# Optimization experiments

Measured on AMD Instinct MI355X. Metric: run time of the kernel, lower is better.

Reference implementation:

```python
import jax, jax.numpy as jnp
import numpy as np
from jax.scipy.linalg import cholesky, solve_triangular, cho_solve

N, M, D = 16384, 2048, 8
VAR, LS = 1.0, 0.5      # RBF kernel hyperparameters (same for kernel_f and kernel_g)
JITTER = 1e-6
BATCH_RATE = 1.0
HALF_LOG_2PI = 0.5 * float(np.log(2.0 * np.pi))


def rbf(x1, x2):
    # K[i,j] = VAR * exp(-||x1_i - x2_j||^2 / (2 LS^2))
    d2 = (jnp.sum(x1 * x1, 1)[:, None] + jnp.sum(x2 * x2, 1)[None, :]
          - 2.0 * (x1 @ x2.T))
    return VAR * jnp.exp(-0.5 * d2 / (LS * LS))


def setup_inputs() -> dict:
    key = jax.random.key(0)
    ks = jax.random.split(key, 7)
    x = jax.random.normal(ks[0], (N, D), dtype=jnp.float32)
    y = jax.random.normal(ks[1], (N, 1), dtype=jnp.float32)
    z = 2.0 * jax.random.uniform(ks[2], (M, D), dtype=jnp.float32) - 1.0  # inducing inputs in [-1,1]^D
    q_m_f = 0.5 * jax.random.normal(ks[3], (M, 1), dtype=jnp.float32)
    q_m_g = 0.5 * jax.random.normal(ks[4], (M, 1), dtype=jnp.float32)
    # Cholesky-like params: identity plus small strictly-lower noise -> PD covariance
    q_L_f = jnp.eye(M, dtype=jnp.float32) + 0.01 * jnp.tril(
        jax.random.normal(ks[5], (M, M), dtype=jnp.float32), -1)
    q_L_g = jnp.eye(M, dtype=jnp.float32) + 0.01 * jnp.tril(
        jax.random.normal(ks[6], (M, M), dtype=jnp.float32), -1)
    return {"x": x, "y": y, "z": z, "q_m_f": q_m_f, "q_L_f": q_L_f,
            "q_m_g": q_m_g, "q_L_g": q_L_g}


def _gp_marginals_and_kl(x, z, q_m, q_L_raw):
    """Marginal posterior mean/var at x and KL(q(u)||p(u)) for one sparse GP."""
    L_S = jnp.tril(q_L_raw)                     # [M,M]
    Kuu = rbf(z, z) + JITTER * jnp.eye(M, dtype=x.dtype)
    Lk = cholesky(Kuu, lower=True)
    Kfu = rbf(x, z)                             # [N,M]
    # A = Kfu @ Kuu^{-1}
    A = cho_solve((Lk, True), Kfu.T).T          # [N,M]
    m = (A @ q_m)[:, 0]                         # [N]
    # diag(Kff + A (S - Kuu) A^T) = diag(Kff) + diag(A S A^T) - diag(Kfu A^T)
    S = L_S @ L_S.T
    diag_Kff = jnp.full((x.shape[0],), VAR, dtype=x.dtype)
    v = diag_Kff + jnp.sum((A @ S) * A, axis=1) - jnp.sum(A * Kfu, axis=1)
    # KL(N(q_m, S) || N(0, Kuu))
    alpha = solve_triangular(Lk, q_m, lower=True)       # Kuu^{-1/2} m
    W = solve_triangular(Lk, L_S, lower=True)           # Kuu^{-1/2} L_S
    logdet_K = 2.0 * jnp.sum(jnp.log(jnp.diag(Lk)))
    logdet_S = 2.0 * jnp.sum(jnp.log(jnp.abs(jnp.diag(L_S))))
    kl = 0.5 * (jnp.sum(W * W) + jnp.sum(alpha * alpha)
                - jnp.asarray(M, x.dtype) + logdet_K - logdet_S)
    return m, v, kl


def reference(x, y, z, q_m_f, q_L_f, q_m_g, q_L_g):
    m_f, v_f, kl_f = _gp_marginals_and_kl(x, z, q_m_f, q_L_f)
    m_g, v_g, kl_g = _gp_marginals_and_kl(x, z, q_m_g, q_L_g)
    yv = y[:, 0]
    # HetGaussian variational expectation (Saul et al. 2016):
    # E_q[log N(y | f, exp(g))] per point
    expectation = (-HALF_LOG_2PI - 0.5 * m_g
                   - 0.5 * ((yv - m_f) ** 2 + v_f) * jnp.exp(-m_g + 0.5 * v_g))
    elbo = BATCH_RATE * jnp.sum(expectation) - (kl_f + kl_g)
    return -elbo
```

## Files before the change

kernel.cpp:

```cpp
#include <hip/hip_runtime.h>
#include <math.h>

#define NN 16384
#define MM 2048
#define DD 8
#define NB 32
#define SZB ((size_t)16777216)

constexpr float HLOG2PI = 0.91893853320467274178f;

using short8  = __attribute__((ext_vector_type(8))) short;
using float4v = __attribute__((ext_vector_type(4))) float;

__device__ __forceinline__ float4v f4zero(){ float4v v; v[0]=0.f; v[1]=0.f; v[2]=0.f; v[3]=0.f; return v; }

__device__ __forceinline__ void bfsplit(float v, short& h, short& lo){
  unsigned b = __float_as_uint(v);
  h = (short)(b >> 16);
  float hf = __uint_as_float(b & 0xFFFF0000u);
  lo = (short)(__float_as_uint(v - hf) >> 16);
}
__device__ __forceinline__ float bf2f(short s){
  return __uint_as_float(((unsigned)(unsigned short)s) << 16);
}
__device__ __forceinline__ float4v mfma3(short8 ah, short8 al, short8 bh, short8 bl, float4v c){
  c = __builtin_amdgcn_mfma_f32_16x16x32_bf16(ah, bh, c, 0, 0, 0);
  c = __builtin_amdgcn_mfma_f32_16x16x32_bf16(ah, bl, c, 0, 0, 0);
  c = __builtin_amdgcn_mfma_f32_16x16x32_bf16(al, bh, c, 0, 0, 0);
  return c;
}

__device__ __forceinline__ float block_reduce(float v, float* scratch){
  int lane = threadIdx.x & 63;
  int w    = threadIdx.x >> 6;
  #pragma unroll
  for (int off=32; off; off>>=1) v += __shfl_down(v, off, 64);
  __syncthreads();
  if (lane==0) scratch[w] = v;
  __syncthreads();
  float r = 0.f;
  if (threadIdx.x < 4) r = scratch[threadIdx.x];
  if (w==0){ r += __shfl_down(r, 2, 64); r += __shfl_down(r, 1, 64); }
  return r;
}

__device__ __forceinline__ void stage64(float (*S)[68], const float* __restrict__ g, int ld, int t){
  #pragma unroll
  for (int p=t; p<1024; p+=256)
    *(float4*)&S[p>>4][(p&15)*4] = *(const float4*)&g[(size_t)(p>>4)*ld + (p&15)*4];
}
__device__ __forceinline__ void tile_gemm_step(float acc[4][4], const float (*As)[68], const float (*Bs)[68], int tx, int ty){
  for (int k=0;k<64;++k){
    float ar[4], bc4[4];
    #pragma unroll
    for (int u=0;u<4;++u){ ar[u]=As[ty*4+u][k]; bc4[u]=Bs[k][tx*4+u]; }
    #pragma unroll
    for (int u=0;u<4;++u)
      #pragma unroll
      for (int v=0;v<4;++v) acc[u][v] += ar[u]*bc4[v];
  }
}
__device__ __forceinline__ void tile_syrk_step(float acc[4][4], const float (*P)[68], const float (*Q)[68], int tx, int ty){
  for (int k=0;k<64;++k){
    float pr[4], qc[4];
    #pragma unroll
    for (int u=0;u<4;++u){ pr[u]=P[ty*4+u][k]; qc[u]=Q[tx*4+u][k]; }
    #pragma unroll
    for (int u=0;u<4;++u)
      #pragma unroll
      for (int v=0;v<4;++v) acc[u][v] += pr[u]*qc[v];
  }
}

__device__ __forceinline__ void factor64_reg(const float (*S)[68],
    float* __restrict__ lkd, float* __restrict__ sdg_, int d, int t){
  if (t < 64){
    float xr[64];
    #pragma unroll
    for (int c4=0;c4<16;++c4) *(float4*)&xr[c4*4] = *(const float4*)&S[t][c4*4];
    float myrp = 1.f;
    #pragma unroll
    for (int j=0;j<64;++j){
      float ajj = __shfl(xr[j], j, 64);
      float piv = sqrtf(fmaxf(ajj, 1e-20f));
      float rp  = 1.f/piv;
      float val = xr[j]*rp;
      if (t==j){ xr[j] = piv; myrp = rp; }
      else if (t>j) xr[j] = val;
      else val = 0.f;
      #pragma unroll
      for (int c=j+1;c<64;++c){
        float vc = __shfl(val, c, 64);
        if (c<=t) xr[c] -= val*vc;
      }
    }
    #pragma unroll
    for (int c=0;c<64;++c) if (c>t) xr[c] = 0.f;
    #pragma unroll
    for (int c4=0;c4<16;++c4)
      *(float4*)&lkd[d*4096 + t*64 + c4*4] = *(float4*)&xr[c4*4];
    sdg_[d*64 + t] = myrp;
  }
}


__global__ __launch_bounds__(256) void phase0_kernel(
    const float* __restrict__ z, float* __restrict__ kuu,
    short* __restrict__ zfh, short* __restrict__ zfl, float* __restrict__ zn2,
    float* __restrict__ lkdiag, float* __restrict__ sdg){
  __shared__ float As[64][68];
  __shared__ float Bs[64][68];
  const int t = threadIdx.x, tx = t & 15, ty = t >> 4;
  const int bid = blockIdx.x;
  if (bid >= 528){
    int zr = (bid-528)*256 + t;
    float v[DD]; float s = 0.f;
    #pragma unroll
    for (int d=0; d<DD; ++d){ v[d] = z[zr*DD + d]; s += v[d]*v[d]; }
    zn2[zr] = s;
    size_t base = (size_t)(zr >> 4)*512 + (zr & 15)*32;
    #pragma unroll
    for (int k=0; k<32; ++k){
      short h = 0, lo = 0;
      if (k < DD) bfsplit(v[k], h, lo);
      zfh[base + k] = h; zfl[base + k] = lo;
    }
    return;
  }
  int idx = bid;
  int r=0; while ((r+1)*(r+2)/2 <= idx) ++r;
  int c = idx - r*(r+1)/2;
  for (int p=t; p<128; p+=256){ int i=p>>1, h=p&1;
    *(float4*)&As[i][h*4] = *(const float4*)&z[(size_t)(r*64+i)*DD + h*4];
    *(float4*)&Bs[i][h*4] = *(const float4*)&z[(size_t)(c*64+i)*DD + h*4]; }
  __syncthreads();
  float kv[4][4];
  #pragma unroll
  for (int u=0;u<4;++u)
    #pragma unroll
    for (int v=0;v<4;++v){
      float d2=0.f;
      #pragma unroll
      for (int d=0;d<8;++d){ float df=As[ty*4+u][d]-Bs[tx*4+v][d]; d2+=df*df; }
      float val = __expf(-2.f*d2);
      if (r*64+ty*4+u == c*64+tx*4+v) val += 1e-6f;
      kv[u][v] = val;
    }
  #pragma unroll
  for (int u=0;u<4;++u)
    *(float4*)&kuu[(size_t)(r*64+ty*4+u)*MM + c*64 + tx*4] =
        make_float4(kv[u][0],kv[u][1],kv[u][2],kv[u][3]);
  if (idx == 0){
    __syncthreads();
    #pragma unroll
    for (int u=0;u<4;++u)
      #pragma unroll
      for (int v=0;v<4;++v) As[ty*4+u][tx*4+v] = kv[u][v];
    __syncthreads();
    factor64_reg(As, lkdiag, sdg, 0, t);
  }
}

__global__ __launch_bounds__(256) void panel_kernel(
    float* __restrict__ kuu, float* __restrict__ lkdiag,
    float* __restrict__ sdg, float* __restrict__ ltri, int kb){
  __shared__ float As[64][68];
  __shared__ float Bs[64][68];
  __shared__ float Cs[64][68];
  __shared__ float sd[64];
  const int t = threadIdx.x, tx = t & 15, ty = t >> 4;
  int idx = blockIdx.x;
  int r=0; while ((r+1)*(r+2)/2 <= idx) ++r;
  int c = idx - r*(r+1)/2;
  int bi = kb+1+r, bc = kb+1+c;
  stage64(Cs, lkdiag + kb*4096, 64, t);
  if (t < 64) sd[t] = sdg[kb*64 + t];
  stage64(As, kuu + (size_t)(bi*64)*MM + kb*64, MM, t);
  if (bc != bi) stage64(Bs, kuu + (size_t)(bc*64)*MM + kb*64, MM, t);
  __syncthreads();
  {
    int w = t>>6, l = t&63;
    if (w==0 || (w==1 && bc!=bi)){
      float (*S)[68] = (w==0)? As : Bs;
      float xr[64];
      #pragma unroll
      for (int c4=0;c4<16;++c4) *(float4*)&xr[c4*4] = *(const float4*)&S[l][c4*4];
      #pragma unroll
      for (int j=0;j<64;++j){
        float xj = xr[j]*sd[j];
        xr[j] = xj;
        #pragma unroll
        for (int cc=j+1;cc<64;++cc) xr[cc] -= xj*Cs[cc][j];
      }
      #pragma unroll
      for (int c4=0;c4<16;++c4) *(float4*)&S[l][c4*4] = *(float4*)&xr[c4*4];
    }
  }
  __syncthreads();
  if (bc == kb+1){
    for (int p=t;p<1024;p+=256)
      *(float4*)&ltri[(size_t)(bi*64+(p>>4))*MM + kb*64 + (p&15)*4] =
          *(float4*)&As[p>>4][(p&15)*4];
  }
  float acc[4][4] = {};
  tile_syrk_step(acc, As, (bc==bi)? As : Bs, tx, ty);
  if (bi==kb+1 && bc==kb+1){
    __syncthreads();
    #pragma unroll
    for (int u=0;u<4;++u)
      #pragma unroll
      for (int v=0;v<4;++v) Bs[ty*4+u][tx*4+v] = acc[u][v];
    __syncthreads();
    for (int p=t;p<1024;p+=256){
      int i=p>>4, c4=p&15;
      float4 kv = *(const float4*)&kuu[(size_t)(bi*64+i)*MM + bi*64 + c4*4];
      float4 bv = *(float4*)&Bs[i][c4*4];
      float4 o; o.x=kv.x-bv.x; o.y=kv.y-bv.y; o.z=kv.z-bv.z; o.w=kv.w-bv.w;
      *(float4*)&As[i][c4*4] = o;
    }
    __syncthreads();
    factor64_reg(As, lkdiag, sdg, kb+1, t);
  } else {
    #pragma unroll
    for (int u=0;u<4;++u){
      float4* dst = (float4*)&kuu[(size_t)(bi*64+ty*4+u)*MM + bc*64 + tx*4];
      float4 o = *dst;
      o.x-=acc[u][0]; o.y-=acc[u][1]; o.z-=acc[u][2]; o.w-=acc[u][3];
      *dst = o;
    }
  }
}

__global__ __launch_bounds__(256) void panel30_phase2_kernel(
    float* __restrict__ kuu, float* __restrict__ lkdiag,
    float* __restrict__ sdg, float* __restrict__ ltri, float* __restrict__ linv){
  __shared__ float As[64][68];
  __shared__ float Bs[64][68];
  __shared__ float Cs[64][68];
  __shared__ float sd[64];
  const int t = threadIdx.x, tx = t & 15, ty = t >> 4;
  const int bid = blockIdx.x;
  int d;
  if (bid == 0){
    const int kb = 30, bi = 31;
    stage64(Cs, lkdiag + kb*4096, 64, t);
    if (t < 64) sd[t] = sdg[kb*64 + t];
    stage64(As, kuu + (size_t)(bi*64)*MM + kb*64, MM, t);
    __syncthreads();
    {
      int w = t>>6, l = t&63;
      if (w==0){
        float xr[64];
        #pragma unroll
        for (int c4=0;c4<16;++c4) *(float4*)&xr[c4*4] = *(const float4*)&As[l][c4*4];
        #pragma unroll
        for (int j=0;j<64;++j){
          float xj = xr[j]*sd[j];
          xr[j] = xj;
          #pragma unroll
          for (int cc=j+1;cc<64;++cc) xr[cc] -= xj*Cs[cc][j];
        }
        #pragma unroll
        for (int c4=0;c4<16;++c4) *(float4*)&As[l][c4*4] = *(float4*)&xr[c4*4];
      }
    }
    __syncthreads();
    for (int p=t;p<1024;p+=256)
      *(float4*)&ltri[(size_t)(bi*64+(p>>4))*MM + kb*64 + (p&15)*4] =
          *(float4*)&As[p>>4][(p&15)*4];
    float acc[4][4] = {};
    tile_syrk_step(acc, As, As, tx, ty);
    __syncthreads();
    #pragma unroll
    for (int u=0;u<4;++u)
      #pragma unroll
      for (int v=0;v<4;++v) Bs[ty*4+u][tx*4+v] = acc[u][v];
    __syncthreads();
    for (int p=t;p<1024;p+=256){
      int i=p>>4, c4=p&15;
      float4 kv = *(const float4*)&kuu[(size_t)(bi*64+i)*MM + bi*64 + c4*4];
      float4 bv = *(float4*)&Bs[i][c4*4];
      float4 o; o.x=kv.x-bv.x; o.y=kv.y-bv.y; o.z=kv.z-bv.z; o.w=kv.w-bv.w;
      *(float4*)&As[i][c4*4] = o;
    }
    __syncthreads();
    factor64_reg(As, lkdiag, sdg, 31, t);
    __syncthreads();
    d = 31;
  } else {
    d = bid - 1;
  }
  stage64(As, lkdiag + d*4096, 64, t);
  __syncthreads();
  if (t < 64){
    for (int j=0;j<64;++j){
      float s = (j==t)?1.f:0.f;
      for (int k=t;k<j;++k) s -= As[j][k]*Bs[k][t];
      Bs[j][t] = (j>=t)? s/As[j][j] : 0.f;
    }
  }
  __syncthreads();
  for (int p=t;p<1024;p+=256){ int i=p>>4, c4=p&15;
    *(float4*)&linv[(size_t)(d*64+i)*MM + d*64 + c4*4] = *(float4*)&Bs[i][c4*4]; }
}

__global__ __launch_bounds__(256) void p3l0_kernel(
    const float* __restrict__ ltri, float* __restrict__ linv){
  __shared__ float As[64][68];
  __shared__ float Bs[64][68];
  const int t = threadIdx.x, tx = t & 15, ty = t >> 4;
  int m = blockIdx.x;
  stage64(As, ltri + (size_t)((2*m+1)*64)*MM + (2*m)*64, MM, t);
  stage64(Bs, linv + (size_t)((2*m)*64)*MM   + (2*m)*64, MM, t);
  __syncthreads();
  float acc[4][4]={};
  tile_gemm_step(acc, As, Bs, tx, ty);
  __syncthreads();
  #pragma unroll
  for (int u=0;u<4;++u)
    #pragma unroll
    for (int v=0;v<4;++v) Bs[ty*4+u][tx*4+v] = acc[u][v];
  stage64(As, linv + (size_t)((2*m+1)*64)*MM + (2*m+1)*64, MM, t);
  __syncthreads();
  float o[4][4]={};
  tile_gemm_step(o, As, Bs, tx, ty);
  #pragma unroll
  for (int u=0;u<4;++u)
    *(float4*)&linv[(size_t)((2*m+1)*64+ty*4+u)*MM + (2*m)*64 + tx*4] =
        make_float4(-o[u][0],-o[u][1],-o[u][2],-o[u][3]);
}

__global__ __launch_bounds__(256) void p3l1_kernel(
    const float* __restrict__ ltri, float* __restrict__ linv, float* __restrict__ ptmp){
  __shared__ float As[64][68];
  __shared__ float Bs[64][68];
  const int t = threadIdx.x, tx = t & 15, ty = t >> 4;
  int m = blockIdx.x;
  float* pm = ptmp + (size_t)m*128*128;
  for (int ti=0; ti<2; ++ti)
    for (int tj=0; tj<2; ++tj){
      int rb = m*4 + 2 + ti, cb0 = m*4;
      float acc[4][4]={};
      for (int k=tj; k<2; ++k){
        __syncthreads();
        stage64(As, ltri + (size_t)(rb*64)*MM + (cb0+k)*64, MM, t);
        stage64(Bs, linv + (size_t)((cb0+k)*64)*MM + (cb0+tj)*64, MM, t);
        __syncthreads();
        tile_gemm_step(acc, As, Bs, tx, ty);
      }
      #pragma unroll
      for (int u=0;u<4;++u)
        *(float4*)&pm[(size_t)(ti*64+ty*4+u)*128 + tj*64 + tx*4] =
            make_float4(acc[u][0],acc[u][1],acc[u][2],acc[u][3]);
    }
  for (int ti=0; ti<2; ++ti)
    for (int tj=0; tj<2; ++tj){
      int rb = m*4 + 2 + ti;
      float acc[4][4]={};
      for (int k=0; k<=ti; ++k){
        __syncthreads();
        stage64(As, linv + (size_t)(rb*64)*MM + (m*4+2+k)*64, MM, t);
        stage64(Bs, pm + (size_t)(k*64)*128 + tj*64, 128, t);
        __syncthreads();
        tile_gemm_step(acc, As, Bs, tx, ty);
      }
      #pragma unroll
      for (int u=0;u<4;++u)
        *(float4*)&linv[(size_t)(rb*64+ty*4+u)*MM + (m*4+tj)*64 + tx*4] =
            make_float4(-acc[u][0],-acc[u][1],-acc[u][2],-acc[u][3]);
    }
}

__global__ __launch_bounds__(256) void p3lA_kernel(
    const float* __restrict__ ltri, const float* __restrict__ linv,
    float* __restrict__ ptmp, int s){
  __shared__ float As[64][68];
  __shared__ float Bs[64][68];
  const int t = threadIdx.x, tx = t & 15, ty = t >> 4;
  int nb = 1<<s, b = 64<<s;
  float* pmb = ptmp + (s==2 ? 131072 : (s==3 ? 393216 : 917504));
  int idx = blockIdx.x;
  int m = idx/(nb*nb), r2 = idx%(nb*nb);
  int ti = r2/nb, tj = r2%nb;
  int rb = m*2*nb + nb + ti, cb0 = m*2*nb;
  float acc[4][4]={};
  for (int k=tj; k<nb; ++k){
    __syncthreads();
    stage64(As, ltri + (size_t)(rb*64)*MM + (cb0+k)*64, MM, t);
    stage64(Bs, linv + (size_t)((cb0+k)*64)*MM + (cb0+tj)*64, MM, t);
    __syncthreads();
    tile_gemm_step(acc, As, Bs, tx, ty);
  }
  float* pm = pmb + (size_t)m*b*b;
  #pragma unroll
  for (int u=0;u<4;++u)
    *(float4*)&pm[(size_t)(ti*64+ty*4+u)*b + tj*64 + tx*4] =
        make_float4(acc[u][0],acc[u][1],acc[u][2],acc[u][3]);
}

__global__ __launch_bounds__(256) void p3lB_kernel(
    float* __restrict__ linv, const float* __restrict__ ptmp, int s){
  __shared__ float As[64][68];
  __shared__ float Bs[64][68];
  const int t = threadIdx.x, tx = t & 15, ty = t >> 4;
  int nb = 1<<s, b = 64<<s;
  const float* pmb = ptmp + (s==2 ? 131072 : (s==3 ? 393216 : 917504));
  int idx = blockIdx.x;
  int m = idx/(nb*nb), r2 = idx%(nb*nb);
  int ti = r2/nb, tj = r2%nb;
  int rb = m*2*nb + nb + ti;
  const float* pm = pmb + (size_t)m*b*b;
  float acc[4][4]={};
  for (int k=0; k<=ti; ++k){
    __syncthreads();
    stage64(As, linv + (size_t)(rb*64)*MM + (m*2*nb+nb+k)*64, MM, t);
    stage64(Bs, pm + (size_t)(k*64)*b + tj*64, b, t);
    __syncthreads();
    tile_gemm_step(acc, As, Bs, tx, ty);
  }
  #pragma unroll
  for (int u=0;u<4;++u)
    *(float4*)&linv[(size_t)(rb*64+ty*4+u)*MM + (m*2*nb+tj)*64 + tx*4] =
        make_float4(-acc[u][0],-acc[u][1],-acc[u][2],-acc[u][3]);
}

__global__ __launch_bounds__(256) void walpha_split_kernel(
    const float* __restrict__ linv, const float* __restrict__ qlf,
    const float* __restrict__ qlg, const float* __restrict__ qmf,
    const float* __restrict__ qmg, float* __restrict__ wf, float* __restrict__ wg,
    float* __restrict__ af, float* __restrict__ ag,
    short* __restrict__ lvh, short* __restrict__ lvl){
  __shared__ float As[64][68];
  __shared__ float Bs[64][68];
  const int t = threadIdx.x, tx = t & 15, ty = t >> 4;
  int idx = blockIdx.x;
  if (idx >= 1312){
    int p = (idx-1312)*256 + t;
    int chunk = p >> 9, wi = p & 511;
    int mo = chunk >> 6, ko = chunk & 63;
    int row = mo*16 + (wi >> 5), col = ko*32 + (wi & 31);
    float v = linv[(size_t)row*MM + col];
    short h, lo; bfsplit(v, h, lo);
    lvh[p] = h; lvl[p] = lo;
    return;
  }
  if (idx >= 1056){
    int abid = idx - 1056;
    int gw = abid*4 + (t>>6), l = t&63;
    for (int job=gw; job<4096; job+=1024){
      int gp = job>>11, r = job&2047;
      const float* qm = gp ? qmg : qmf;
      float s=0.f;
      for (int c=l; c<=r; c+=64) s += linv[(size_t)r*MM+c]*qm[c];
      #pragma unroll
      for (int off=32; off; off>>=1) s += __shfl_down(s, off, 64);
      if (l==0) (gp ? ag : af)[r] = s;
    }
    return;
  }
  int gp = idx/528, rem = idx%528;
  int bi=0; while ((bi+1)*(bi+2)/2 <= rem) ++bi;
  int bj = rem - bi*(bi+1)/2;
  const float* ql = gp ? qlg : qlf;
  float* w        = gp ? wg  : wf;
  float acc[4][4]={};
  for (int bk=bj; bk<=bi; ++bk){
    __syncthreads();
    stage64(As, linv + (size_t)(bi*64)*MM + bk*64, MM, t);
    stage64(Bs, ql   + (size_t)(bk*64)*MM + bj*64, MM, t);
    __syncthreads();
    if (bk==bj){
      for (int p=t;p<4096;p+=256){ int i=p>>6, c=p&63; if (i<c) Bs[i][c]=0.f; }
      __syncthreads();
    }
    tile_gemm_step(acc, As, Bs, tx, ty);
  }
  #pragma unroll
  for (int u=0;u<4;++u)
    *(float4*)&w[(size_t)(bi*64+ty*4+u)*MM + bj*64 + tx*4] =
        make_float4(acc[u][0],acc[u][1],acc[u][2],acc[u][3]);
}

__global__ __launch_bounds__(256) void reduce_kernel(
    const float* __restrict__ lkd, const float* __restrict__ qlf,
    const float* __restrict__ qlg, const float* __restrict__ af,
    const float* __restrict__ ag, const float* __restrict__ wf,
    const float* __restrict__ wg, float* __restrict__ scal){
  __shared__ float scratch[4];
  if (blockIdx.x == 512){
    float ldk=0, ldf=0, ldg=0, a2f=0, a2g=0;
    for (int i=threadIdx.x;i<MM;i+=256){
      int kb = i>>6, r = i&63;
      ldk += __logf(lkd[kb*4096 + r*64 + r]);
      ldf += __logf(fabsf(qlf[(size_t)i*MM+i]));
      ldg += __logf(fabsf(qlg[(size_t)i*MM+i]));
      float v = af[i]; a2f += v*v;
      v = ag[i];       a2g += v*v;
    }
    float r;
    r = block_reduce(ldk, scratch); if (threadIdx.x==0) scal[0] = 2.f*r;
    r = block_reduce(ldf, scratch); if (threadIdx.x==0) scal[1] = 2.f*r;
    r = block_reduce(ldg, scratch); if (threadIdx.x==0) scal[2] = 2.f*r;
    r = block_reduce(a2f, scratch); if (threadIdx.x==0) scal[3] = r;
    r = block_reduce(a2g, scratch); if (threadIdx.x==0) scal[4] = r;
    return;
  }
  size_t start  = (size_t)blockIdx.x*256 + threadIdx.x;
  size_t stride = (size_t)512*256;
  float sf=0, sg=0;
  for (size_t p=start;p<(size_t)MM*MM;p+=stride){
    float v=wf[p]; sf += v*v;
    v=wg[p];       sg += v*v;
  }
  float r = block_reduce(sf, scratch);
  if (threadIdx.x==0) atomicAdd(&scal[5], r);
  r = block_reduce(sg, scratch);
  if (threadIdx.x==0) atomicAdd(&scal[6], r);
}

__global__ __launch_bounds__(256, 2) void split_tt_kernel(
    const float* __restrict__ wf, const float* __restrict__ wg,
    short* __restrict__ wfh, short* __restrict__ wfl,
    short* __restrict__ wgh, short* __restrict__ wgl,
    const float* __restrict__ x, const float* __restrict__ zn2,
    const short* __restrict__ zfh, const short* __restrict__ zfl,
    const short* __restrict__ lvh, const short* __restrict__ lvl,
    short* __restrict__ tth, short* __restrict__ ttl){
  __shared__ __align__(16) short lAh[8192], lAl[8192], lBh[8192], lBl[8192];
  __shared__ float tile[32][33];
  const int t = threadIdx.x;
  const int bid = blockIdx.x;
  if (bid < 8192){
    int zz = bid >> 12;
    int rem = bid & 4095;
    int mb = rem & 63, kb = rem >> 6;
    const float* src = zz ? wg : wf;
    short* dh = zz ? wgh : wfh;
    short* dl = zz ? wgl : wfl;
    #pragma unroll
    for (int k=0;k<4;++k){
      int idx = t + k*256;
      int lr = idx >> 5, lc = idx & 31;
      tile[lr][lc] = src[(size_t)(kb*32+lr)*MM + mb*32 + lc];
    }
    __syncthreads();
    #pragma unroll
    for (int e=0;e<4;++e){
      int p = t*4 + e;
      int c = p >> 9, wi = p & 511;
      int i = (wi >> 5) & 15, kk = wi & 31;
      float v = tile[kk][c*16 + i];
      short h, lo; bfsplit(v, h, lo);
      size_t gp = ((size_t)(mb*2 + c)*64 + kb)*512 + wi;
      dh[gp] = h; dl[gp] = lo;
    }
    return;
  }
  int v0 = bid - 8192;
  int istrip = v0 % 128, bj2 = v0 / 128;
  int l = t & 63, w = t >> 6;
  int li = l & 15, q = l >> 4;
  int lofs = li*32 + q*8;
  int lofs_s = li*32 + ((q ^ ((li>>1)&3)))*8;
  int wn4 = (w>>1)*4, wm4 = (w&1)*4;

  short8 xh[2], xl[2];
  float xn2v[8];
  {
    float xn2t[2];
    #pragma unroll
    for (int tn=0; tn<2; ++tn){
      int n = istrip*128 + w*32 + tn*16 + li;
      const float4* xp = (const float4*)(x + (size_t)n*DD);
      float4 p0 = xp[0], p1 = xp[1];
      float v[8] = {p0.x,p0.y,p0.z,p0.w,p1.x,p1.y,p1.z,p1.w};
      float s = 0.f;
      #pragma unroll
      for (int d=0; d<8; ++d) s += v[d]*v[d];
      xn2t[tn] = s;
      short8 hh, ll;
      #pragma unroll
      for (int j=0; j<8; ++j){
        short h=0, lo=0;
        if (q==0) bfsplit(v[j], h, lo);
        hh[j]=h; ll[j]=lo;
      }
      xh[tn]=hh; xl[tn]=ll;
    }
    #pragma unroll
    for (int tn=0; tn<2; ++tn)
      #pragma unroll
      for (int r=0; r<4; ++r)
        xn2v[tn*4+r] = __shfl(xn2t[tn], q*4 + r, 64);
  }

  float4v acc[4][4];
  #pragma unroll
  for (int i=0;i<4;++i)
    #pragma unroll
    for (int j=0;j<4;++j) acc[i][j] = f4zero();

  int nkt = 2*bj2 + 2;
  for (int bk=0; bk<nkt; ++bk){
    __syncthreads();
    {
      short8 zh[4], zl[4];
      float zt2[4];
      #pragma unroll
      for (int tz=0; tz<4; ++tz){
        size_t zo = (size_t)(bk*4 + tz)*512 + lofs;
        zh[tz] = *(const short8*)(zfh + zo);
        zl[tz] = *(const short8*)(zfl + zo);
        zt2[tz] = zn2[bk*64 + tz*16 + li];
      }
      #pragma unroll
      for (int tn=0; tn<2; ++tn){
        #pragma unroll
        for (int tz=0; tz<4; ++tz){
          float4v s4 = mfma3(xh[tn], xl[tn], zh[tz], zl[tz], f4zero());
          #pragma unroll
          for (int r=0; r<4; ++r){
            float e = __expf(4.f*s4[r] - 2.f*(xn2v[tn*4+r] + zt2[tz]));
            short h, lo; bfsplit(e, h, lo);
            int rowc = q*4 + r;
            int slot2 = (((tz&1)*2 + (li>>3)) ^ ((rowc>>1)&3));
            int pos = ((w*2+tn)*2 + (tz>>1))*512 + rowc*32 + slot2*8 + (li&7);
            lAh[pos] = h; lAl[pos] = lo;
          }
        }
      }
    }
    #pragma unroll
    for (int c4 = t; c4 < 1024; c4 += 256){
      int ch = c4 >> 6, wdi = c4 & 63;
      int wsw = (wdi & 60) | ((wdi ^ (wdi >> 3)) & 3);
      int dst = ch*64 + wsw;
      size_t g = ((size_t)(bj2*8 + (ch>>1))*64 + (size_t)(bk*2 + (ch&1)))*64 + wdi;
      ((uint4*)lBh)[dst] = ((const uint4*)lvh)[g];
      ((uint4*)lBl)[dst] = ((const uint4*)lvl)[g];
    }
    __syncthreads();
    #pragma unroll
    for (int s=0; s<2; ++s){
      short8 ah[4], al[4], bh[4], bl[4];
      #pragma unroll
      for (int tn=0; tn<4; ++tn){
        int off = ((wn4+tn)*2 + s)*512 + lofs_s;
        ah[tn] = *(const short8*)&lAh[off];
        al[tn] = *(const short8*)&lAl[off];
      }
      #pragma unroll
      for (int tm=0; tm<4; ++tm){
        int off = ((wm4+tm)*2 + s)*512 + lofs_s;
        bh[tm] = *(const short8*)&lBh[off];
        bl[tm] = *(const short8*)&lBl[off];
      }
      #pragma unroll
      for (int tn=0; tn<4; ++tn)
        #pragma unroll
        for (int tm=0; tm<4; ++tm)
          acc[tn][tm] = mfma3(ah[tn], al[tn], bh[tm], bl[tm], acc[tn][tm]);
    }
  }
  #pragma unroll
  for (int tn=0; tn<4; ++tn){
    int no_g = istrip*8 + wn4 + tn;
    #pragma unroll
    for (int tm=0; tm<4; ++tm){
      int mo_g = bj2*4 + (w&1)*2 + (tm>>1);
      size_t cb = ((size_t)no_g*64 + mo_g)*512;
      #pragma unroll
      for (int r=0; r<4; ++r){
        short h, lo; bfsplit(acc[tn][tm][r], h, lo);
        size_t pos = cb + (q*4+r)*32 + (tm&1)*16 + li;
        tth[pos] = h; ttl[pos] = lo;
      }
    }
  }
}

__global__ __launch_bounds__(256, 2) void linquadkl_kernel(
    const short* __restrict__ tth, const short* __restrict__ ttl,
    const float* __restrict__ af, const float* __restrict__ ag,
    float* __restrict__ t2, float* __restrict__ lf, float* __restrict__ lg,
    const short* __restrict__ wfh, const short* __restrict__ wfl,
    const short* __restrict__ wgh, const short* __restrict__ wgl,
    float* __restrict__ vfq, float* __restrict__ vgq,
    const float* __restrict__ scal, float* __restrict__ out){
  __shared__ __align__(16) short lAh[8192], lAl[8192], lBh[8192], lBl[8192];
  const int t = threadIdx.x;
  const int bid = blockIdx.x;
  if (bid == 8192){
    if (t == 0){
      float klf = 0.5f*(scal[5] + scal[3] - (float)MM + scal[0] - scal[1]);
      float klg = 0.5f*(scal[6] + scal[4] - (float)MM + scal[0] - scal[2]);
      out[0] += klf + klg;
    }
    return;
  }
  if (bid < 4096){
    int w = t >> 6, l = t & 63;
    int n = bid*4 + w;
    int g = l >> 2, j = l & 3;
    float s2=0.f, sf=0.f, sg=0.f;
    #pragma unroll
    for (int it=0; it<4; ++it){
      int ck = g + it*16;
      size_t off = ((size_t)(n>>4)*64 + ck)*512 + (n&15)*32 + j*8;
      short8 h8 = *(const short8*)(tth + off);
      short8 l8 = *(const short8*)(ttl + off);
      int m0 = ck*32 + j*8;
      float4 a0 = *(const float4*)(af + m0), a1 = *(const float4*)(af + m0 + 4);
      float4 g0 = *(const float4*)(ag + m0), g1 = *(const float4*)(ag + m0 + 4);
      float av[8] = {a0.x,a0.y,a0.z,a0.w,a1.x,a1.y,a1.z,a1.w};
      float gv[8] = {g0.x,g0.y,g0.z,g0.w,g1.x,g1.y,g1.z,g1.w};
      #pragma unroll
      for (int e=0; e<8; ++e){
        float tv = bf2f(h8[e]) + bf2f(l8[e]);
        s2 += tv*tv; sf += tv*av[e]; sg += tv*gv[e];
      }
    }
    #pragma unroll
    for (int off=32; off; off>>=1){
      s2 += __shfl_down(s2, off, 64);
      sf += __shfl_down(sf, off, 64);
      sg += __shfl_down(sg, off, 64);
    }
    if (l==0){ t2[n] = s2; lf[n] = sf; lg[n] = sg; }
    return;
  }
  int v0 = bid - 4096;
  int istrip = v0 % 128, bj2 = (v0 / 128) % 16, zz = v0 / 2048;
  int l = t & 63, w = t >> 6;
  const short* gbh = zz ? wgh : wfh;
  const short* gbl = zz ? wgl : wfl;
  float* vq = zz ? vgq : vfq;
  int li = l & 15, q = l >> 4;
  int lofs_s = li*32 + ((q ^ ((li>>1)&3)))*8;
  int wn4 = (w>>1)*4, wm4 = (w&1)*4;

  float4v acc[4][4];
  #pragma unroll
  for (int i=0;i<4;++i)
    #pragma unroll
    for (int j=0;j<4;++j) acc[i][j] = f4zero();

  for (int bk=2*bj2; bk<32; ++bk){
    __syncthreads();
    #pragma unroll
    for (int c4 = t; c4 < 1024; c4 += 256){
      int ch = c4 >> 6, wdi = c4 & 63;
      int wsw = (wdi & 60) | ((wdi ^ (wdi >> 3)) & 3);
      int dst = ch*64 + wsw;
      size_t ga = ((size_t)(istrip*8 + (ch>>1))*64 + (size_t)(bk*2 + (ch&1)))*64 + wdi;
      ((uint4*)lAh)[dst] = ((const uint4*)tth)[ga];
      ((uint4*)lAl)[dst] = ((const uint4*)ttl)[ga];
      size_t gb = ((size_t)(bj2*8 + (ch>>1))*64 + (size_t)(bk*2 + (ch&1)))*64 + wdi;
      ((uint4*)lBh)[dst] = ((const uint4*)gbh)[gb];
      ((uint4*)lBl)[dst] = ((const uint4*)gbl)[gb];
    }
    __syncthreads();
    #pragma unroll
    for (int s=0; s<2; ++s){
      short8 ah[4], al[4], bh[4], bl[4];
      #pragma unroll
      for (int tn=0; tn<4; ++tn){
        int off = ((wn4+tn)*2 + s)*512 + lofs_s;
        ah[tn] = *(const short8*)&lAh[off];
        al[tn] = *(const short8*)&lAl[off];
      }
      #pragma unroll
      for (int tm=0; tm<4; ++tm){
        int off = ((wm4+tm)*2 + s)*512 + lofs_s;
        bh[tm] = *(const short8*)&lBh[off];
        bl[tm] = *(const short8*)&lBl[off];
      }
      #pragma unroll
      for (int tn=0; tn<4; ++tn)
        #pragma unroll
        for (int tm=0; tm<4; ++tm)
          acc[tn][tm] = mfma3(ah[tn], al[tn], bh[tm], bl[tm], acc[tn][tm]);
    }
  }
  float rs[16];
  #pragma unroll
  for (int tn=0; tn<4; ++tn)
    #pragma unroll
    for (int r=0; r<4; ++r){
      float s = 0.f;
      #pragma unroll
      for (int tm=0; tm<4; ++tm){ float v = acc[tn][tm][r]; s += v*v; }
      rs[tn*4+r] = s;
    }
  #pragma unroll
  for (int off=8; off; off>>=1)
    #pragma unroll
    for (int k=0; k<16; ++k) rs[k] += __shfl_down(rs[k], off, 16);
  if (li == 0){
    #pragma unroll
    for (int tn=0; tn<4; ++tn)
      #pragma unroll
      for (int r=0; r<4; ++r){
        int n = istrip*128 + (w>>1)*64 + tn*16 + q*4 + r;
        atomicAdd(&vq[n], rs[tn*4+r]);
      }
  }
}

__global__ __launch_bounds__(256) void final_kernel(const float* __restrict__ y,
    const float* __restrict__ t2, const float* __restrict__ lf, const float* __restrict__ lg,
    const float* __restrict__ vfq, const float* __restrict__ vgq, float* __restrict__ out){
  __shared__ float scratch[4];
  int i = blockIdx.x*256 + threadIdx.x;
  float mf = lf[i], mg = lg[i];
  float vf = 1.f + vfq[i] - t2[i];
  float vg = 1.f + vgq[i] - t2[i];
  float dy = y[i] - mf;
  float e = -HLOG2PI - 0.5f*mg - 0.5f*(dy*dy + vf)*__expf(-mg + 0.5f*vg);
  float r = block_reduce(e, scratch);
  if (threadIdx.x==0) atomicAdd(out, -r);
}

extern "C" void kernel_launch(void* const* d_in, const int* in_sizes, int n_in,
                              void* d_out, int out_size, void* d_ws, size_t ws_size,
                              hipStream_t stream){
  (void)in_sizes; (void)n_in; (void)out_size; (void)ws_size;
  const float* x   = (const float*)d_in[0];
  const float* y   = (const float*)d_in[1];
  const float* z   = (const float*)d_in[2];
  const float* qmf = (const float*)d_in[3];
  const float* qlf = (const float*)d_in[4];
  const float* qmg = (const float*)d_in[5];
  const float* qlg = (const float*)d_in[6];
  float* out = (float*)d_out;
  char* Bw = (char*)d_ws;

  float* kuu  = (float*)Bw;
  float* linv = (float*)(Bw + SZB);
  float* wf   = (float*)(Bw + 2*SZB);
  float* wg   = (float*)(Bw + 3*SZB);
  short* lvh  = (short*)Bw;
  short* lvl  = (short*)(Bw + SZB/2);
  short* wfh  = (short*)(Bw + SZB);
  short* wfl  = (short*)(Bw + SZB + SZB/2);
  short* wgh  = (short*)(Bw + 2*SZB);
  short* wgl  = (short*)(Bw + 2*SZB + SZB/2);
  short* tth  = (short*)(Bw + 3*SZB);
  short* ttl  = (short*)(Bw + 3*SZB + (size_t)NN*MM*2);
  float* ltri   = (float*)(Bw + 4*SZB);
  float* ptmp   = (float*)(Bw + 5*SZB);
  float* lkdiag = (float*)(Bw + 5*SZB + (size_t)8388608);
  float* sdg    = (float*)(Bw + 5*SZB + (size_t)8388608 + (size_t)524288);
  float* sm   = (float*)(Bw + 3*SZB + (size_t)NN*MM*4);
  float* af = sm;          float* ag = af + MM;
  float* t2 = ag + MM;     float* lf = t2 + NN;   float* lg = lf + NN;
  float* vfq = lg + NN;    float* vgq = vfq + NN; float* scal = vgq + NN;
  float* zn2 = scal + 64 + 2048;
  short* zfh = (short*)(zn2 + MM);
  short* zfl = zfh + MM*32;

  hipMemsetAsync(out, 0, sizeof(float), stream);
  hipMemsetAsync(vfq, 0, (size_t)(2*NN + 64 + 2048)*sizeof(float), stream);
  hipMemsetAsync(wf,  0, 2*SZB, stream);
  hipMemsetAsync(linv,0, SZB,   stream);

  phase0_kernel<<<536, 256, 0, stream>>>(z, kuu, zfh, zfl, zn2, lkdiag, sdg);
  for (int kb = 0; kb < 30; ++kb){
    int T = NB - 1 - kb;
    panel_kernel<<<T*(T+1)/2, 256, 0, stream>>>(kuu, lkdiag, sdg, ltri, kb);
  }
  panel30_phase2_kernel<<<32, 256, 0, stream>>>(kuu, lkdiag, sdg, ltri, linv);
  p3l0_kernel<<<16, 256, 0, stream>>>(ltri, linv);
  p3l1_kernel<<<8, 256, 0, stream>>>(ltri, linv, ptmp);
  for (int s = 2; s < 5; ++s){
    int nb = 1<<s, mc = 16>>s;
    p3lA_kernel<<<mc*nb*nb, 256, 0, stream>>>(ltri, linv, ptmp, s);
    p3lB_kernel<<<mc*nb*nb, 256, 0, stream>>>(linv, ptmp, s);
  }
  walpha_split_kernel<<<17696, 256, 0, stream>>>(linv, qlf, qlg, qmf, qmg,
                                                 wf, wg, af, ag, lvh, lvl);
  reduce_kernel<<<513, 256, 0, stream>>>(lkdiag, qlf, qlg, af, ag, wf, wg, scal);
  split_tt_kernel<<<10240, 256, 0, stream>>>(wf, wg, wfh, wfl, wgh, wgl,
                                             x, zn2, zfh, zfl, lvh, lvl, tth, ttl);
  linquadkl_kernel<<<8193, 256, 0, stream>>>(tth, ttl, af, ag, t2, lf, lg,
                                             wfh, wfl, wgh, wgl, vfq, vgq, scal, out);
  final_kernel<<<NN/256, 256, 0, stream>>>(y, t2, lf, lg, vfq, vgq, out);
}
```

Baseline: 3.827 ms.

## Fuse two Cholesky panel steps per launch to halve kernel launches

Replaces the 30 per-column-block panel launches of the blocked Cholesky with 15 launches, each handling two 64-wide column blocks. Every block redundantly factors the second diagonal block and applies both trailing updates before writing back. This removes half of the serialized launches and one global read-modify-write of the trailing matrix per pair. In exchange each block does redundant factorization work and uses more shared memory (six 64x68 tiles), which may reduce occupancy.

```diff
diff --git a/kernel.cpp b/kernel.cpp
--- a/kernel.cpp
+++ b/kernel.cpp
@@ -70,6 +70,20 @@
       #pragma unroll
       for (int v=0;v<4;++v) acc[u][v] += pr[u]*qc[v];
   }
+}
+__device__ __forceinline__ void trsm_row(float* Srow, const float (*C)[68], const float* sdv){
+  float xr[64];
+  #pragma unroll
+  for (int c4=0;c4<16;++c4) *(float4*)&xr[c4*4] = *(const float4*)&Srow[c4*4];
+  #pragma unroll
+  for (int j=0;j<64;++j){
+    float xj = xr[j]*sdv[j];
+    xr[j] = xj;
+    #pragma unroll
+    for (int cc=j+1;cc<64;++cc) xr[cc] -= xj*C[cc][j];
+  }
+  #pragma unroll
+  for (int c4=0;c4<16;++c4) *(float4*)&Srow[c4*4] = *(float4*)&xr[c4*4];
 }
 
 __device__ __forceinline__ void factor64_reg(const float (*S)[68],
@@ -100,6 +114,42 @@
     for (int c4=0;c4<16;++c4)
       *(float4*)&lkd[d*4096 + t*64 + c4*4] = *(float4*)&xr[c4*4];
     sdg_[d*64 + t] = myrp;
+  }
+}
+
+__device__ __forceinline__ void factor64_ip(float (*S)[68], float* sdl,
+    float* __restrict__ lkd, float* __restrict__ sdg_, int d, int t, bool glob){
+  if (t < 64){
+    float xr[64];
+    #pragma unroll
+    for (int c4=0;c4<16;++c4) *(float4*)&xr[c4*4] = *(const float4*)&S[t][c4*4];
+    float myrp = 1.f;
+    #pragma unroll
+    for (int j=0;j<64;++j){
+      float ajj = __shfl(xr[j], j, 64);
+      float piv = sqrtf(fmaxf(ajj, 1e-20f));
+      float rp  = 1.f/piv;
+      float val = xr[j]*rp;
+      if (t==j){ xr[j] = piv; myrp = rp; }
+      else if (t>j) xr[j] = val;
+      else val = 0.f;
+      #pragma unroll
+      for (int c=j+1;c<64;++c){
+        float vc = __shfl(val, c, 64);
+        if (c<=t) xr[c] -= val*vc;
+      }
+    }
+    #pragma unroll
+    for (int c=0;c<64;++c) if (c>t) xr[c] = 0.f;
+    #pragma unroll
+    for (int c4=0;c4<16;++c4) *(float4*)&S[t][c4*4] = *(float4*)&xr[c4*4];
+    sdl[t] = myrp;
+    if (glob){
+      #pragma unroll
+      for (int c4=0;c4<16;++c4)
+        *(float4*)&lkd[d*4096 + t*64 + c4*4] = *(float4*)&xr[c4*4];
+      sdg_[d*64 + t] = myrp;
+    }
   }
 }
 
@@ -161,71 +211,112 @@
   }
 }
 
-__global__ __launch_bounds__(256) void panel_kernel(
+__global__ __launch_bounds__(256) void panel2_kernel(
     float* __restrict__ kuu, float* __restrict__ lkdiag,
-    float* __restrict__ sdg, float* __restrict__ ltri, int kb){
+    float* __restrict__ sdg, float* __restrict__ ltri, int p){
   __shared__ float As[64][68];
   __shared__ float Bs[64][68];
+  __shared__ float A1s[64][68];
+  __shared__ float B1s[64][68];
   __shared__ float Cs[64][68];
-  __shared__ float sd[64];
+  __shared__ float Ds[64][68];
+  __shared__ float sd[64], sd2[64];
   const int t = threadIdx.x, tx = t & 15, ty = t >> 4;
+  const int d0 = 2*p, d1 = 2*p+1, rs = 2*p+2;
   int idx = blockIdx.x;
   int r=0; while ((r+1)*(r+2)/2 <= idx) ++r;
   int c = idx - r*(r+1)/2;
-  int bi = kb+1+r, bc = kb+1+c;
-  stage64(Cs, lkdiag + kb*4096, 64, t);
-  if (t < 64) sd[t] = sdg[kb*64 + t];
-  stage64(As, kuu + (size_t)(bi*64)*MM + kb*64, MM, t);
-  if (bc != bi) stage64(Bs, kuu + (size_t)(bc*64)*MM + kb*64, MM, t);
+  int bi = rs + r, bc = rs + c;
+  const bool dual = (bc != bi);
+  stage64(Cs, lkdiag + d0*4096, 64, t);
+  if (t < 64) sd[t] = sdg[d0*64 + t];
+  stage64(As, kuu + (size_t)(bi*64)*MM + d0*64, MM, t);
+  if (dual) stage64(Bs, kuu + (size_t)(bc*64)*MM + d0*64, MM, t);
+  stage64(Ds, kuu + (size_t)(d1*64)*MM + d0*64, MM, t);
   __syncthreads();
   {
     int w = t>>6, l = t&63;
-    if (w==0 || (w==1 && bc!=bi)){
-      float (*S)[68] = (w==0)? As : Bs;
-      float xr[64];
-      #pragma unroll
-      for (int c4=0;c4<16;++c4) *(float4*)&xr[c4*4] = *(const float4*)&S[l][c4*4];
-      #pragma unroll
-      for (int j=0;j<64;++j){
-        float xj = xr[j]*sd[j];
-        xr[j] = xj;
-        #pragma unroll
-        for (int cc=j+1;cc<64;++cc) xr[cc] -= xj*Cs[cc][j];
-      }
-      #pragma unroll
-      for (int c4=0;c4<16;++c4) *(float4*)&S[l][c4*4] = *(float4*)&xr[c4*4];
-    }
-  }
-  __syncthreads();
-  if (bc == kb+1){
-    for (int p=t;p<1024;p+=256)
-      *(float4*)&ltri[(size_t)(bi*64+(p>>4))*MM + kb*64 + (p&15)*4] =
-          *(float4*)&As[p>>4][(p&15)*4];
-  }
-  float acc[4][4] = {};
-  tile_syrk_step(acc, As, (bc==bi)? As : Bs, tx, ty);
-  if (bi==kb+1 && bc==kb+1){
-    __syncthreads();
+    float (*S)[68] = (w==0) ? As : ((w==1 && dual) ? Bs : ((w==2) ? Ds : (float(*)[68])nullptr));
+    if (S) trsm_row(&S[l][0], (const float (*)[68])Cs, sd);
+  }
+  __syncthreads();
+  if (bc == rs){
+    for (int q=t;q<1024;q+=256)
+      *(float4*)&ltri[(size_t)(bi*64+(q>>4))*MM + d0*64 + (q&15)*4] =
+          *(float4*)&As[q>>4][(q&15)*4];
+  }
+  if (idx == 0){
+    for (int q=t;q<1024;q+=256)
+      *(float4*)&ltri[(size_t)(d1*64+(q>>4))*MM + d0*64 + (q&15)*4] =
+          *(float4*)&Ds[q>>4][(q&15)*4];
+  }
+  {
+    float accd[4][4] = {};
+    tile_syrk_step(accd, (const float (*)[68])Ds, (const float (*)[68])Ds, tx, ty);
+    #pragma unroll
+    for (int u=0;u<4;++u){
+      float4 kv = *(const float4*)&kuu[(size_t)(d1*64+ty*4+u)*MM + d1*64 + tx*4];
+      Cs[ty*4+u][tx*4  ] = kv.x - accd[u][0];
+      Cs[ty*4+u][tx*4+1] = kv.y - accd[u][1];
+      Cs[ty*4+u][tx*4+2] = kv.z - accd[u][2];
+      Cs[ty*4+u][tx*4+3] = kv.w - accd[u][3];
+    }
+  }
+  __syncthreads();
+  factor64_ip(Cs, sd2, lkdiag, sdg, d1, t, (idx==0));
+  stage64(A1s, kuu + (size_t)(bi*64)*MM + d1*64, MM, t);
+  if (dual) stage64(B1s, kuu + (size_t)(bc*64)*MM + d1*64, MM, t);
+  __syncthreads();
+  {
+    float aA[4][4]={}, aB[4][4]={};
+    tile_syrk_step(aA, (const float (*)[68])As, (const float (*)[68])Ds, tx, ty);
+    if (dual) tile_syrk_step(aB, (const float (*)[68])Bs, (const float (*)[68])Ds, tx, ty);
     #pragma unroll
     for (int u=0;u<4;++u)
       #pragma unroll
-      for (int v=0;v<4;++v) Bs[ty*4+u][tx*4+v] = acc[u][v];
-    __syncthreads();
-    for (int p=t;p<1024;p+=256){
-      int i=p>>4, c4=p&15;
-      float4 kv = *(const float4*)&kuu[(size_t)(bi*64+i)*MM + bi*64 + c4*4];
-      float4 bv = *(float4*)&Bs[i][c4*4];
-      float4 o; o.x=kv.x-bv.x; o.y=kv.y-bv.y; o.z=kv.z-bv.z; o.w=kv.w-bv.w;
-      *(float4*)&As[i][c4*4] = o;
-    }
-    __syncthreads();
-    factor64_reg(As, lkdiag, sdg, kb+1, t);
+      for (int v=0;v<4;++v){
+        A1s[ty*4+u][tx*4+v] -= aA[u][v];
+        if (dual) B1s[ty*4+u][tx*4+v] -= aB[u][v];
+      }
+  }
+  __syncthreads();
+  {
+    int w = t>>6, l = t&63;
+    float (*S)[68] = (w==0) ? A1s : ((w==1 && dual) ? B1s : (float(*)[68])nullptr);
+    if (S) trsm_row(&S[l][0], (const float (*)[68])Cs, sd2);
+  }
+  __syncthreads();
+  if (bc == rs){
+    for (int q=t;q<1024;q+=256)
+      *(float4*)&ltri[(size_t)(bi*64+(q>>4))*MM + d1*64 + (q&15)*4] =
+          *(float4*)&A1s[q>>4][(q&15)*4];
+  }
+  float acc0[4][4]={}, acc1[4][4]={};
+  tile_syrk_step(acc0, (const float (*)[68])As,  dual ? (const float (*)[68])Bs  : (const float (*)[68])As,  tx, ty);
+  tile_syrk_step(acc1, (const float (*)[68])A1s, dual ? (const float (*)[68])B1s : (const float (*)[68])A1s, tx, ty);
+  if (idx == 0){
+    __syncthreads();
+    #pragma unroll
+    for (int u=0;u<4;++u){
+      float4 kv = *(const float4*)&kuu[(size_t)(rs*64+ty*4+u)*MM + rs*64 + tx*4];
+      float x0 = kv.x - acc0[u][0]; x0 -= acc1[u][0];
+      float x1 = kv.y - acc0[u][1]; x1 -= acc1[u][1];
+      float x2 = kv.z - acc0[u][2]; x2 -= acc1[u][2];
+      float x3 = kv.w - acc0[u][3]; x3 -= acc1[u][3];
+      Bs[ty*4+u][tx*4  ] = x0;
+      Bs[ty*4+u][tx*4+1] = x1;
+      Bs[ty*4+u][tx*4+2] = x2;
+      Bs[ty*4+u][tx*4+3] = x3;
+    }
+    __syncthreads();
+    factor64_reg((const float (*)[68])Bs, lkdiag, sdg, rs, t);
   } else {
     #pragma unroll
     for (int u=0;u<4;++u){
       float4* dst = (float4*)&kuu[(size_t)(bi*64+ty*4+u)*MM + bc*64 + tx*4];
       float4 o = *dst;
-      o.x-=acc[u][0]; o.y-=acc[u][1]; o.z-=acc[u][2]; o.w-=acc[u][3];
+      o.x-=acc0[u][0]; o.y-=acc0[u][1]; o.z-=acc0[u][2]; o.w-=acc0[u][3];
+      o.x-=acc1[u][0]; o.y-=acc1[u][1]; o.z-=acc1[u][2]; o.w-=acc1[u][3];
       *dst = o;
     }
   }
@@ -249,27 +340,14 @@
     __syncthreads();
     {
       int w = t>>6, l = t&63;
-      if (w==0){
-        float xr[64];
-        #pragma unroll
-        for (int c4=0;c4<16;++c4) *(float4*)&xr[c4*4] = *(const float4*)&As[l][c4*4];
-        #pragma unroll
-        for (int j=0;j<64;++j){
-          float xj = xr[j]*sd[j];
-          xr[j] = xj;
-          #pragma unroll
-          for (int cc=j+1;cc<64;++cc) xr[cc] -= xj*Cs[cc][j];
-        }
-        #pragma unroll
-        for (int c4=0;c4<16;++c4) *(float4*)&As[l][c4*4] = *(float4*)&xr[c4*4];
-      }
+      if (w==0) trsm_row(&As[l][0], (const float (*)[68])Cs, sd);
     }
     __syncthreads();
     for (int p=t;p<1024;p+=256)
       *(float4*)&ltri[(size_t)(bi*64+(p>>4))*MM + kb*64 + (p&15)*4] =
           *(float4*)&As[p>>4][(p&15)*4];
     float acc[4][4] = {};
-    tile_syrk_step(acc, As, As, tx, ty);
+    tile_syrk_step(acc, (const float (*)[68])As, (const float (*)[68])As, tx, ty);
     __syncthreads();
     #pragma unroll
     for (int u=0;u<4;++u)
@@ -284,7 +362,7 @@
       *(float4*)&As[i][c4*4] = o;
     }
     __syncthreads();
-    factor64_reg(As, lkdiag, sdg, 31, t);
+    factor64_reg((const float (*)[68])As, lkdiag, sdg, 31, t);
     __syncthreads();
     d = 31;
   } else {
@@ -314,7 +392,7 @@
   stage64(Bs, linv + (size_t)((2*m)*64)*MM   + (2*m)*64, MM, t);
   __syncthreads();
   float acc[4][4]={};
-  tile_gemm_step(acc, As, Bs, tx, ty);
+  tile_gemm_step(acc, (const float (*)[68])As, (const float (*)[68])Bs, tx, ty);
   __syncthreads();
   #pragma unroll
   for (int u=0;u<4;++u)
@@ -323,7 +401,7 @@
   stage64(As, linv + (size_t)((2*m+1)*64)*MM + (2*m+1)*64, MM, t);
   __syncthreads();
   float o[4][4]={};
-  tile_gemm_step(o, As, Bs, tx, ty);
+  tile_gemm_step(o, (const float (*)[68])As, (const float (*)[68])Bs, tx, ty);
   #pragma unroll
   for (int u=0;u<4;++u)
     *(float4*)&linv[(size_t)((2*m+1)*64+ty*4+u)*MM + (2*m)*64 + tx*4] =
@@ -346,7 +424,7 @@
         stage64(As, ltri + (size_t)(rb*64)*MM + (cb0+k)*64, MM, t);
         stage64(Bs, linv + (size_t)((cb0+k)*64)*MM + (cb0+tj)*64, MM, t);
         __syncthreads();
-        tile_gemm_step(acc, As, Bs, tx, ty);
+        tile_gemm_step(acc, (const float (*)[68])As, (const float (*)[68])Bs, tx, ty);
       }
       #pragma unroll
       for (int u=0;u<4;++u)
@@ -362,7 +440,7 @@
         stage64(As, linv + (size_t)(rb*64)*MM + (m*4+2+k)*64, MM, t);
         stage64(Bs, pm + (size_t)(k*64)*128 + tj*64, 128, t);
         __syncthreads();
-        tile_gemm_step(acc, As, Bs, tx, ty);
+        tile_gemm_step(acc, (const float (*)[68])As, (const float (*)[68])Bs, tx, ty);
       }
       #pragma unroll
       for (int u=0;u<4;++u)
@@ -389,7 +467,7 @@
     stage64(As, ltri + (size_t)(rb*64)*MM + (cb0+k)*64, MM, t);
     stage64(Bs, linv + (size_t)((cb0+k)*64)*MM + (cb0+tj)*64, MM, t);
     __syncthreads();
-    tile_gemm_step(acc, As, Bs, tx, ty);
+    tile_gemm_step(acc, (const float (*)[68])As, (const float (*)[68])Bs, tx, ty);
   }
   float* pm = pmb + (size_t)m*b*b;
   #pragma unroll
@@ -416,7 +494,7 @@
     stage64(As, linv + (size_t)(rb*64)*MM + (m*2*nb+nb+k)*64, MM, t);
     stage64(Bs, pm + (size_t)(k*64)*b + tj*64, b, t);
     __syncthreads();
-    tile_gemm_step(acc, As, Bs, tx, ty);
+    tile_gemm_step(acc, (const float (*)[68])As, (const float (*)[68])Bs, tx, ty);
   }
   #pragma unroll
   for (int u=0;u<4;++u)
@@ -473,7 +551,7 @@
       for (int p=t;p<4096;p+=256){ int i=p>>6, c=p&63; if (i<c) Bs[i][c]=0.f; }
       __syncthreads();
     }
-    tile_gemm_step(acc, As, Bs, tx, ty);
+    tile_gemm_step(acc, (const float (*)[68])As, (const float (*)[68])Bs, tx, ty);
   }
   #pragma unroll
   for (int u=0;u<4;++u)
@@ -865,9 +943,9 @@
   hipMemsetAsync(linv,0, SZB,   stream);
 
   phase0_kernel<<<536, 256, 0, stream>>>(z, kuu, zfh, zfl, zn2, lkdiag, sdg);
-  for (int kb = 0; kb < 30; ++kb){
-    int T = NB - 1 - kb;
-    panel_kernel<<<T*(T+1)/2, 256, 0, stream>>>(kuu, lkdiag, sdg, ltri, kb);
+  for (int p = 0; p < 15; ++p){
+    int T = 30 - 2*p;
+    panel2_kernel<<<T*(T+1)/2, 256, 0, stream>>>(kuu, lkdiag, sdg, ltri, p);
   }
   panel30_phase2_kernel<<<32, 256, 0, stream>>>(kuu, lkdiag, sdg, ltri, linv);
   p3l0_kernel<<<16, 256, 0, stream>>>(ltri, linv);
```

New measurement: 3.992 ms. +4.3%, slower.
